# Kernel tuning notes

Hardware: AMD Instinct MI355X
Metric: run time of the kernel (lower is better)

The kernel has to match this reference:

```python
import jax, jax.numpy as jnp
import numpy as np

N, C_IN, C_OUT, F, K = 4, 16, 16, 500000, 5


def setup_inputs() -> dict:
    key = jax.random.key(0)
    k1, k2, k3 = jax.random.split(key, 3)
    x = jax.random.normal(k1, (N, C_IN, F, K), dtype=jnp.float32)
    # Conv2d weight layout OIHW: (out_channels, in_channels, 1, k)
    W = jax.random.normal(k2, (C_OUT, C_IN, 1, K), dtype=jnp.float32) * 0.05
    b = jax.random.normal(k3, (C_OUT,), dtype=jnp.float32) * 0.05
    return {"x": x, "W": W, "b": b}


def reference(x, W, b):
    # x: (N, C, F, 5); symmetric neighbor combine (MeshCNN-style)
    x0 = x[:, :, :, 0]
    x1 = x[:, :, :, 1] + x[:, :, :, 3]
    x2 = x[:, :, :, 2] + x[:, :, :, 4]
    x3 = jnp.abs(x[:, :, :, 1] - x[:, :, :, 3])
    x4 = jnp.abs(x[:, :, :, 2] - x[:, :, :, 4])
    # stack at dim=2 (as in source): (N, C, 5, F)
    g = jnp.stack([x0, x1, x2, x3, x4], axis=2)
    # Conv2d kernel (1, k), VALID padding -> (N, C_out, 5, F - k + 1)
    y = jax.lax.conv_general_dilated(
        g, W, window_strides=(1, 1), padding="VALID",
        dimension_numbers=("NCHW", "OIHW", "NCHW"))
    return y + b[None, :, None, None]
```

## Files before the change

### kernel.cpp

```cpp
#include <hip/hip_runtime.h>
#include <hip/hip_bf16.h>


constexpr int NN   = 4;
constexpr int CIN  = 16;
constexpr int COUT = 16;
constexpr int FF   = 500000;
constexpr int KK   = 5;
constexpr int FO   = FF - 4;
constexpr int TF   = 64;
constexpr int TFH  = TF + 4;

__global__ __launch_bounds__(256, 2)
void meshconv_kernel(const float* __restrict__ x,
                     const float* __restrict__ W,
                     const float* __restrict__ b,
                     float* __restrict__ out)
{
    __shared__ float g_lds[CIN * TFH * 5];

    const int n  = blockIdx.y;
    const int w0 = blockIdx.x * TF;
    const int t  = threadIdx.x;

    for (int p = t; p < CIN * TFH; p += 256) {
        const int i  = p / TFH;
        const int fl = p - i * TFH;
        const int f  = w0 + fl;
        float x0 = 0.f, x1 = 0.f, x2 = 0.f, x3 = 0.f, x4 = 0.f;
        if (f < FF) {
            const float* xp = x + ((n * CIN + i) * (size_t)FF + f) * KK;
            x0 = xp[0]; x1 = xp[1]; x2 = xp[2]; x3 = xp[3]; x4 = xp[4];
        }
        float* gp = g_lds + p * 5;
        gp[0] = x0;
        gp[1] = x1 + x3;
        gp[2] = x2 + x4;
        gp[3] = fabsf(x1 - x3);
        gp[4] = fabsf(x2 - x4);
    }
    __syncthreads();

    const int wl = t & 63;
    const int og = __builtin_amdgcn_readfirstlane(t >> 6);
    const int w  = w0 + wl;

    float acc[5][4];
    #pragma unroll
    for (int h = 0; h < 5; ++h)
        #pragma unroll
        for (int oo = 0; oo < 4; ++oo) acc[h][oo] = 0.f;

    for (int i = 0; i < CIN; ++i) {
        float ws[4][5];
        #pragma unroll
        for (int oo = 0; oo < 4; ++oo)
            #pragma unroll
            for (int kw = 0; kw < KK; ++kw)
                ws[oo][kw] = W[((og * 4 + oo) * CIN + i) * KK + kw];

        const float* gi = g_lds + (i * TFH + wl) * 5;
        #pragma unroll
        for (int kw = 0; kw < KK; ++kw) {
            float gh[5];
            #pragma unroll
            for (int h = 0; h < 5; ++h) gh[h] = gi[kw * 5 + h];
            #pragma unroll
            for (int oo = 0; oo < 4; ++oo)
                #pragma unroll
                for (int h = 0; h < 5; ++h)
                    acc[h][oo] = fmaf(ws[oo][kw], gh[h], acc[h][oo]);
        }
    }

    if (w < FO) {
        #pragma unroll
        for (int oo = 0; oo < 4; ++oo) {
            const int o = og * 4 + oo;
            const float bias = b[o];
            #pragma unroll
            for (int h = 0; h < 5; ++h)
                out[((n * COUT + o) * 5 + h) * (size_t)FO + w] = acc[h][oo] + bias;
        }
    }
}

extern "C" void kernel_launch(void* const* d_in, const int* in_sizes, int n_in,
                              void* d_out, int out_size, void* d_ws, size_t ws_size,
                              hipStream_t stream)
{
    const float* x = (const float*)d_in[0];
    const float* W = (const float*)d_in[1];
    const float* b = (const float*)d_in[2];
    float* out = (float*)d_out;

    const int ntiles = (FO + TF - 1) / TF;
    dim3 grid(ntiles, NN);
    dim3 block(256);
    meshconv_kernel<<<grid, block, 0, stream>>>(x, W, b, out);
}
```

Measured before the change: 1.125 ms.

## Use single-wave blocks computing all 16 outputs with packed FP32 FMA

Shrinks the block from 256 to 64 threads, so each thread computes all 16 output channels for its column instead of 4. The inner product now uses 2-wide float vectors so the compiler can emit packed FMA instructions, and the bias is folded into the accumulator initialisation. Each column's 25 LDS values are loaded once per input channel and reused across all outputs, cutting redundant LDS reads. In exchange the per-thread register count rises sharply (80 accumulators plus the loaded values) and each block now loads its tile with a quarter of the threads, which may reduce latency hiding on this memory-bound kernel.

```diff
diff --git a/kernel.cpp b/kernel.cpp
--- a/kernel.cpp
+++ b/kernel.cpp
@@ -1,6 +1,7 @@
 #include <hip/hip_runtime.h>
-#include <hip/hip_bf16.h>
 
+
+using f32x2 = __attribute__((ext_vector_type(2))) float;
 
 constexpr int NN   = 4;
 constexpr int CIN  = 16;
@@ -11,7 +12,7 @@
 constexpr int TF   = 64;
 constexpr int TFH  = TF + 4;
 
-__global__ __launch_bounds__(256, 2)
+__global__ __launch_bounds__(64)
 void meshconv_kernel(const float* __restrict__ x,
                      const float* __restrict__ W,
                      const float* __restrict__ b,
@@ -23,7 +24,7 @@
     const int w0 = blockIdx.x * TF;
     const int t  = threadIdx.x;
 
-    for (int p = t; p < CIN * TFH; p += 256) {
+    for (int p = t; p < CIN * TFH; p += 64) {
         const int i  = p / TFH;
         const int fl = p - i * TFH;
         const int f  = w0 + fl;
@@ -41,46 +42,59 @@
     }
     __syncthreads();
 
-    const int wl = t & 63;
-    const int og = __builtin_amdgcn_readfirstlane(t >> 6);
-    const int w  = w0 + wl;
-
-    float acc[5][4];
+    f32x2 acc[5][8];
     #pragma unroll
     for (int h = 0; h < 5; ++h)
         #pragma unroll
-        for (int oo = 0; oo < 4; ++oo) acc[h][oo] = 0.f;
+        for (int j = 0; j < 8; ++j)
+            acc[h][j] = f32x2{b[2 * j], b[2 * j + 1]};
 
+    const int wl = t;
+
+    #pragma unroll 2
     for (int i = 0; i < CIN; ++i) {
-        float ws[4][5];
+        const float* gi = g_lds + (i * TFH + wl) * 5;
+        float g25[25];
         #pragma unroll
-        for (int oo = 0; oo < 4; ++oo)
+        for (int q = 0; q < 25; ++q) g25[q] = gi[q];
+
+        #pragma unroll
+        for (int half = 0; half < 2; ++half) {
+            f32x2 ws[4][5];
+            #pragma unroll
+            for (int j = 0; j < 4; ++j)
+                #pragma unroll
+                for (int kw = 0; kw < KK; ++kw) {
+                    const int o0 = half * 8 + 2 * j;
+                    ws[j][kw] = f32x2{W[((o0    ) * CIN + i) * KK + kw],
+                                      W[((o0 + 1) * CIN + i) * KK + kw]};
+                }
+
             #pragma unroll
             for (int kw = 0; kw < KK; ++kw)
-                ws[oo][kw] = W[((og * 4 + oo) * CIN + i) * KK + kw];
-
-        const float* gi = g_lds + (i * TFH + wl) * 5;
-        #pragma unroll
-        for (int kw = 0; kw < KK; ++kw) {
-            float gh[5];
-            #pragma unroll
-            for (int h = 0; h < 5; ++h) gh[h] = gi[kw * 5 + h];
-            #pragma unroll
-            for (int oo = 0; oo < 4; ++oo)
                 #pragma unroll
-                for (int h = 0; h < 5; ++h)
-                    acc[h][oo] = fmaf(ws[oo][kw], gh[h], acc[h][oo]);
+                for (int h = 0; h < 5; ++h) {
+                    const float gv = g25[kw * 5 + h];
+                    const f32x2 gg = {gv, gv};
+                    #pragma unroll
+                    for (int j = 0; j < 4; ++j)
+                        acc[h][half * 4 + j] =
+                            __builtin_elementwise_fma(ws[j][kw], gg,
+                                                      acc[h][half * 4 + j]);
+                }
         }
     }
 
+    const int w = w0 + wl;
     if (w < FO) {
         #pragma unroll
-        for (int oo = 0; oo < 4; ++oo) {
-            const int o = og * 4 + oo;
-            const float bias = b[o];
+        for (int j = 0; j < 8; ++j) {
+            const int o = 2 * j;
             #pragma unroll
-            for (int h = 0; h < 5; ++h)
-                out[((n * COUT + o) * 5 + h) * (size_t)FO + w] = acc[h][oo] + bias;
+            for (int h = 0; h < 5; ++h) {
+                out[((n * COUT + o    ) * 5 + h) * (size_t)FO + w] = acc[h][j].x;
+                out[((n * COUT + o + 1) * 5 + h) * (size_t)FO + w] = acc[h][j].y;
+            }
         }
     }
 }
@@ -96,6 +110,6 @@
 
     const int ntiles = (FO + TF - 1) / TF;
     dim3 grid(ntiles, NN);
-    dim3 block(256);
+    dim3 block(64);
     meshconv_kernel<<<grid, block, 0, stream>>>(x, W, b, out);
 }
```

After: 1.311 ms. +16.5%, slower.
